# Kernel tuning notes

Measured on AMD Instinct MI355X. Metric: run time of the kernel, lower is better.

Reference implementation:

```python
import jax, jax.numpy as jnp
from jax import lax
import numpy as np

BATCH = 131072
D_IN = 512
D_OUT = 512
ITERS = 10
THRES = 1e-6


def bjorck_orthonormalize(w, iters=ITERS, thres=THRES):
    """Order-1 Bjorck orthonormalization: W <- 1.5*W - 0.5*W (W^T W).

    Row-orthogonal if out<=in, column-orthogonal otherwise (operate on W^T).
    Early-stops when max|delta| <= thres, matching the module's tolerance.
    """
    transpose = w.shape[0] > w.shape[1]
    if transpose:
        w = w.T

    def cond(state):
        i, _, err = state
        return jnp.logical_and(i < iters, err > thres)

    def body(state):
        i, w, _ = state
        w_new = 1.5 * w - 0.5 * (w @ (w.T @ w))
        err = jnp.max(jnp.abs(w_new - w))
        return i + 1, w_new, err

    _, w, _ = lax.while_loop(
        cond, body, (jnp.array(0, jnp.int32), w, jnp.array(jnp.inf, w.dtype))
    )
    if transpose:
        w = w.T
    return w


def setup_inputs() -> dict:
    key = jax.random.key(0)
    k1, k2 = jax.random.split(key)
    inputs = jax.random.normal(k1, (BATCH, D_IN), dtype=jnp.float32)
    # scaled Gaussian so singular values lie in (0, sqrt(3)) -> Bjorck converges
    weight = jax.random.normal(k2, (D_OUT, D_IN), dtype=jnp.float32) * (0.5 / np.sqrt(D_IN))
    return {"inputs": inputs, "weight": weight}


def reference(inputs, weight):
    # training-mode forward with projection=True, inverse=False:
    # weight.data <- bjorck(weight.data); out = F.linear(inputs, weight)
    w_proj = bjorck_orthonormalize(weight)
    return inputs @ w_proj.T  # [batch, out_features]
```

## Files before the change

### kernel.cpp

```cpp
#include <hip/hip_runtime.h>


using bf16x8 = __attribute__((ext_vector_type(8))) short;
using f32x4  = __attribute__((ext_vector_type(4))) float;
using u16x8  = __attribute__((ext_vector_type(8))) unsigned short;

#define DI 512
#define MFMA16(a, b, c) __builtin_amdgcn_mfma_f32_16x16x32_bf16(a, b, c, 0, 0, 0)
#define SXS 520

__device__ __forceinline__ unsigned short f2bf(float f) {
  unsigned int u = __builtin_bit_cast(unsigned int, f);
  u += 0x7FFFu + ((u >> 16) & 1u);
  return (unsigned short)(u >> 16);
}
__device__ __forceinline__ float bf2f(unsigned short h) {
  unsigned int u = ((unsigned int)h) << 16;
  return __builtin_bit_cast(float, u);
}

__global__ void k_split(const float* __restrict__ W, float* __restrict__ Wm,
                        unsigned short* __restrict__ Wh, unsigned short* __restrict__ Wl,
                        unsigned short* __restrict__ WTh, unsigned short* __restrict__ WTl) {
  int idx = blockIdx.x * blockDim.x + threadIdx.x;
  int m = idx >> 9, i = idx & 511;
  float w = W[idx];
  Wm[idx] = w;
  unsigned short h  = f2bf(w);
  unsigned short lo = f2bf(w - bf2f(h));
  Wh[idx] = h; Wl[idx] = lo;
  WTh[i * DI + m] = h; WTl[i * DI + m] = lo;
}

__global__ __launch_bounds__(256) void k_mm2(
    const unsigned short* __restrict__ Ah, const unsigned short* __restrict__ Al,
    const unsigned short* __restrict__ Bh, const unsigned short* __restrict__ Bl,
    int mode,
    const float* __restrict__ Wm_in, float* __restrict__ Wm_out,
    unsigned short* __restrict__ Oh, unsigned short* __restrict__ Ol,
    unsigned short* __restrict__ OTh, unsigned short* __restrict__ OTl) {
  const int tid = threadIdx.x;
  const int l = tid & 63, lw = tid >> 6;
  const int wid = (blockIdx.x << 2) | lw;
  const int tile = wid >> 1, half = wid & 1;
  const int m0 = (tile >> 5) << 4, n0 = (tile & 31) << 4;
  const int kb = half << 8;
  const int lm = l & 15, lk = l >> 4;
  const int ra = (m0 + lm) * DI + kb + (lk << 3);
  const int rb = (n0 + lm) * DI + kb + (lk << 3);

  __shared__ f32x4 red[2][64];
  const int pr = lw >> 1;

  f32x4 a0{}, a1{}, a2{}, a3{}, a4{}, a5{};
#pragma unroll
  for (int k0 = 0; k0 < 256; k0 += 64) {
    bf16x8 ah0 = *(const bf16x8*)&Ah[ra + k0];
    bf16x8 al0 = *(const bf16x8*)&Al[ra + k0];
    bf16x8 bh0 = *(const bf16x8*)&Bh[rb + k0];
    bf16x8 bl0 = *(const bf16x8*)&Bl[rb + k0];
    bf16x8 ah1 = *(const bf16x8*)&Ah[ra + k0 + 32];
    bf16x8 al1 = *(const bf16x8*)&Al[ra + k0 + 32];
    bf16x8 bh1 = *(const bf16x8*)&Bh[rb + k0 + 32];
    bf16x8 bl1 = *(const bf16x8*)&Bl[rb + k0 + 32];
    a0 = MFMA16(ah0, bh0, a0);
    a1 = MFMA16(ah0, bl0, a1);
    a2 = MFMA16(al0, bh0, a2);
    a3 = MFMA16(ah1, bh1, a3);
    a4 = MFMA16(ah1, bl1, a4);
    a5 = MFMA16(al1, bh1, a5);
  }
  f32x4 acc = (a0 + a1) + (a2 + a3) + (a4 + a5);

  if (half) red[pr][l] = acc;
  __syncthreads();
  if (!half) {
    acc += red[pr][l];
    const int r0 = m0 + (lk << 2);
    const int cn = n0 + lm;
#pragma unroll
    for (int r = 0; r < 4; ++r) {
      const int gm = r0 + r, gn = cn;
      const float v = acc[r];
      if (mode == 0) {
        unsigned short h = f2bf(v);
        Oh[gm * DI + gn] = h;
        Ol[gm * DI + gn] = f2bf(v - bf2f(h));
      } else if (mode == 1) {
        const float wn = 1.5f * Wm_in[gm * DI + gn] - 0.5f * v;
        Wm_out[gm * DI + gn] = wn;
        unsigned short h = f2bf(wn), lo = f2bf(wn - bf2f(h));
        Oh[gm * DI + gn] = h;   Ol[gm * DI + gn] = lo;
        OTh[gn * DI + gm] = h;  OTl[gn * DI + gm] = lo;
      } else {
        const float wn = 1.5f * Wm_in[gm * DI + gn] - 0.5f * v;
        Oh[gm * DI + gn] = f2bf(wn);
      }
    }
  }
}

#if defined(__has_builtin)
#if __has_builtin(__builtin_amdgcn_global_load_lds)
#define HAVE_GLDS 1
#endif
#endif

#ifdef HAVE_GLDS
__device__ __forceinline__ void gl2lds16(const unsigned short* g, unsigned short* lds) {
  __builtin_amdgcn_global_load_lds(
      (const __attribute__((address_space(1))) void*)g,
      (__attribute__((address_space(3))) void*)lds, 16, 0, 0);
}
#endif

__global__ __launch_bounds__(512, 1) void k_big(
    const float* __restrict__ X, const unsigned short* __restrict__ Wp,
    float* __restrict__ out) {
  __shared__ unsigned short sX[64 * SXS];
  __shared__ unsigned short sB[2][512 * 32];
  const int tid = threadIdx.x;
  const int wv = tid >> 6, l = tid & 63;
  const int lm = l & 15, lk = l >> 4;
  const int ck = lk ^ ((lm >> 1) & 3);
  const int wm = wv >> 2, wn = wv & 3;
  const int rowbase = blockIdx.x << 6;

  const int srow = l >> 2;
  const int scs = (l & 3) ^ ((srow >> 1) & 3);
  auto stage_b = [&](int kk, int bb) {
#pragma unroll
    for (int p = 0; p < 4; ++p) {
      const int rowblk = (wv << 6) + (p << 4);
      const unsigned short* src = &Wp[(rowblk + srow) * DI + (kk << 5) + (scs << 3)];
#ifdef HAVE_GLDS
      gl2lds16(src, &sB[bb][rowblk << 5]);
#else
      *(u16x8*)&sB[bb][(rowblk << 5) + l * 8] = *(const u16x8*)src;
#endif
    }
  };

  stage_b(0, 0);
  {
    const int xrow = tid >> 3;
    const int ci = tid & 7;
    const float* xp = &X[(rowbase + xrow) * DI];
#pragma unroll
    for (int i = 0; i < 8; ++i) {
      const int c_abs = ci + (i << 3);
      f32x4 v0 = *(const f32x4*)(xp + c_abs * 8);
      f32x4 v1 = *(const f32x4*)(xp + c_abs * 8 + 4);
      u16x8 h;
      h[0] = f2bf(v0[0]); h[1] = f2bf(v0[1]); h[2] = f2bf(v0[2]); h[3] = f2bf(v0[3]);
      h[4] = f2bf(v1[0]); h[5] = f2bf(v1[1]); h[6] = f2bf(v1[2]); h[7] = f2bf(v1[3]);
      *(u16x8*)&sX[xrow * SXS + c_abs * 8] = h;
    }
  }
  __syncthreads();

  f32x4 acc[2][8] = {};
  for (int k = 0; k < 16; ++k) {
    const int buf = k & 1;
    if (k < 15) stage_b(k + 1, buf ^ 1);
    bf16x8 a[2], b[8];
#pragma unroll
    for (int mf = 0; mf < 2; ++mf)
      a[mf] = *(const bf16x8*)&sX[((wm << 5) + (mf << 4) + lm) * SXS + (k << 5) + (lk << 3)];
#pragma unroll
    for (int nf = 0; nf < 8; ++nf)
      b[nf] = *(const bf16x8*)&sB[buf][(((wn << 7) + (nf << 4) + lm) << 5) + (ck << 3)];
#pragma unroll
    for (int mf = 0; mf < 2; ++mf)
#pragma unroll
      for (int nf = 0; nf < 8; ++nf)
        acc[mf][nf] = MFMA16(b[nf], a[mf], acc[mf][nf]);
    __syncthreads();
  }

#pragma unroll
  for (int mf = 0; mf < 2; ++mf) {
    const int gm = rowbase + (wm << 5) + (mf << 4) + lm;
#pragma unroll
    for (int nf = 0; nf < 8; ++nf) {
      const int gn = (wn << 7) + (nf << 4) + (lk << 2);
      *(f32x4*)&out[gm * DI + gn] = acc[mf][nf];
    }
  }
}

extern "C" void kernel_launch(void* const* d_in, const int* in_sizes, int n_in,
                              void* d_out, int out_size, void* d_ws, size_t ws_size,
                              hipStream_t stream) {
  const float* X = (const float*)d_in[0];
  const float* W = (const float*)d_in[1];
  float* out = (float*)d_out;

  char* ws = (char*)d_ws;
  size_t off = 0;
  auto carve = [&](size_t bytes) { void* p = ws + off; off += (bytes + 255) & ~(size_t)255; return p; };

  const size_t F32 = (size_t)DI * DI * 4;
  const size_t BF  = (size_t)DI * DI * 2;

  float* Wm[2];           unsigned short *Wh[2], *Wl[2], *WTh[2], *WTl[2];
  Wm[0]  = (float*)carve(F32);          Wm[1]  = (float*)carve(F32);
  Wh[0]  = (unsigned short*)carve(BF);  Wh[1]  = (unsigned short*)carve(BF);
  Wl[0]  = (unsigned short*)carve(BF);  Wl[1]  = (unsigned short*)carve(BF);
  WTh[0] = (unsigned short*)carve(BF);  WTh[1] = (unsigned short*)carve(BF);
  WTl[0] = (unsigned short*)carve(BF);  WTl[1] = (unsigned short*)carve(BF);
  unsigned short* Gh = (unsigned short*)carve(BF);
  unsigned short* Gl = (unsigned short*)carve(BF);

  k_split<<<1024, 256, 0, stream>>>(W, Wm[0], Wh[0], Wl[0], WTh[0], WTl[0]);

  int cur = 0;
  for (int it = 0; it < 10; ++it) {
    k_mm2<<<512, 256, 0, stream>>>(WTh[cur], WTl[cur], WTh[cur], WTl[cur], 0,
                                   nullptr, nullptr, Gh, Gl, nullptr, nullptr);
    const int nxt = cur ^ 1;
    k_mm2<<<512, 256, 0, stream>>>(Wh[cur], Wl[cur], Gh, Gl, (it == 9) ? 2 : 1,
                                   Wm[cur], Wm[nxt], Wh[nxt], Wl[nxt], WTh[nxt], WTl[nxt]);
    cur = nxt;
  }

  k_big<<<2048, 512, 0, stream>>>(X, Wh[cur], out);
}
```

Before: 429.1 us.

## Read weight fragments directly from global memory in big GEMM, drop LDS staging

The main GEMM kernel stops staging the projected weight through double-buffered shared memory with async global-to-LDS loads. Each wave now loads its 64-column weight slice straight from global (L2-resident) memory, and the wave tiling changes from 2x8 to 4x4 fragments per wave. Per-k-step barriers go away, and the launch bounds are raised so more blocks can be resident. The cost is more global or L2 traffic for the weight, since each block rereads it without sharing through LDS, and load latency is now exposed inside the MFMA loop.

```diff
diff --git a/kernel.cpp b/kernel.cpp
--- a/kernel.cpp
+++ b/kernel.cpp
@@ -100,90 +100,56 @@
   }
 }
 
-#if defined(__has_builtin)
-#if __has_builtin(__builtin_amdgcn_global_load_lds)
-#define HAVE_GLDS 1
-#endif
-#endif
-
-#ifdef HAVE_GLDS
-__device__ __forceinline__ void gl2lds16(const unsigned short* g, unsigned short* lds) {
-  __builtin_amdgcn_global_load_lds(
-      (const __attribute__((address_space(1))) void*)g,
-      (__attribute__((address_space(3))) void*)lds, 16, 0, 0);
-}
-#endif
-
-__global__ __launch_bounds__(512, 1) void k_big(
+__global__ __launch_bounds__(512, 4) void k_big(
     const float* __restrict__ X, const unsigned short* __restrict__ Wp,
     float* __restrict__ out) {
   __shared__ unsigned short sX[64 * SXS];
-  __shared__ unsigned short sB[2][512 * 32];
   const int tid = threadIdx.x;
   const int wv = tid >> 6, l = tid & 63;
   const int lm = l & 15, lk = l >> 4;
-  const int ck = lk ^ ((lm >> 1) & 3);
-  const int wm = wv >> 2, wn = wv & 3;
   const int rowbase = blockIdx.x << 6;
 
-  const int srow = l >> 2;
-  const int scs = (l & 3) ^ ((srow >> 1) & 3);
-  auto stage_b = [&](int kk, int bb) {
-#pragma unroll
-    for (int p = 0; p < 4; ++p) {
-      const int rowblk = (wv << 6) + (p << 4);
-      const unsigned short* src = &Wp[(rowblk + srow) * DI + (kk << 5) + (scs << 3)];
-#ifdef HAVE_GLDS
-      gl2lds16(src, &sB[bb][rowblk << 5]);
-#else
-      *(u16x8*)&sB[bb][(rowblk << 5) + l * 8] = *(const u16x8*)src;
-#endif
-    }
-  };
-
-  stage_b(0, 0);
   {
     const int xrow = tid >> 3;
     const int ci = tid & 7;
     const float* xp = &X[(rowbase + xrow) * DI];
 #pragma unroll
     for (int i = 0; i < 8; ++i) {
-      const int c_abs = ci + (i << 3);
-      f32x4 v0 = *(const f32x4*)(xp + c_abs * 8);
-      f32x4 v1 = *(const f32x4*)(xp + c_abs * 8 + 4);
+      const int c = ci + (i << 3);
+      f32x4 v0 = *(const f32x4*)(xp + c * 8);
+      f32x4 v1 = *(const f32x4*)(xp + c * 8 + 4);
       u16x8 h;
       h[0] = f2bf(v0[0]); h[1] = f2bf(v0[1]); h[2] = f2bf(v0[2]); h[3] = f2bf(v0[3]);
       h[4] = f2bf(v1[0]); h[5] = f2bf(v1[1]); h[6] = f2bf(v1[2]); h[7] = f2bf(v1[3]);
-      *(u16x8*)&sX[xrow * SXS + c_abs * 8] = h;
+      *(u16x8*)&sX[xrow * SXS + c * 8] = h;
     }
   }
   __syncthreads();
 
-  f32x4 acc[2][8] = {};
+  f32x4 acc[4][4] = {};
+  const unsigned short* wbase = &Wp[(((wv << 6) + lm) * DI) + (lk << 3)];
+#pragma unroll 4
   for (int k = 0; k < 16; ++k) {
-    const int buf = k & 1;
-    if (k < 15) stage_b(k + 1, buf ^ 1);
-    bf16x8 a[2], b[8];
+    bf16x8 b[4], a[4];
 #pragma unroll
-    for (int mf = 0; mf < 2; ++mf)
-      a[mf] = *(const bf16x8*)&sX[((wm << 5) + (mf << 4) + lm) * SXS + (k << 5) + (lk << 3)];
+    for (int nf = 0; nf < 4; ++nf)
+      b[nf] = *(const bf16x8*)&wbase[((nf << 4) * DI) + (k << 5)];
 #pragma unroll
-    for (int nf = 0; nf < 8; ++nf)
-      b[nf] = *(const bf16x8*)&sB[buf][(((wn << 7) + (nf << 4) + lm) << 5) + (ck << 3)];
+    for (int mf = 0; mf < 4; ++mf)
+      a[mf] = *(const bf16x8*)&sX[((mf << 4) + lm) * SXS + (k << 5) + (lk << 3)];
 #pragma unroll
-    for (int mf = 0; mf < 2; ++mf)
+    for (int mf = 0; mf < 4; ++mf)
 #pragma unroll
-      for (int nf = 0; nf < 8; ++nf)
+      for (int nf = 0; nf < 4; ++nf)
         acc[mf][nf] = MFMA16(b[nf], a[mf], acc[mf][nf]);
-    __syncthreads();
   }
 
 #pragma unroll
-  for (int mf = 0; mf < 2; ++mf) {
-    const int gm = rowbase + (wm << 5) + (mf << 4) + lm;
+  for (int mf = 0; mf < 4; ++mf) {
+    const int gm = rowbase + (mf << 4) + lm;
 #pragma unroll
-    for (int nf = 0; nf < 8; ++nf) {
-      const int gn = (wn << 7) + (nf << 4) + (lk << 2);
+    for (int nf = 0; nf < 4; ++nf) {
+      const int gn = (wv << 6) + (nf << 4) + (lk << 2);
       *(f32x4*)&out[gm * DI + gn] = acc[mf][nf];
     }
   }
```

After: 423.1 us. No clear change (-1.4%).
